# Kernel optimization log

Hardware: AMD Instinct MI355X
Metric: run time of the kernel (lower is better)

The kernel has to match this reference:

```python
import jax, jax.numpy as jnp
import numpy as np

STRIDE = (1, 1)
PAD = (1, 1)

def setup_inputs() -> dict:
    key = jax.random.key(0)
    k1, k2, k3 = jax.random.split(key, 3)
    x = jax.random.normal(k1, (32, 128, 56, 56), dtype=jnp.float32)
    # K ~ N(0,1) per nn.init.normal_(self.K)
    K = jax.random.normal(k2, (256, 128, 3, 3), dtype=jnp.float32)
    bias = jax.random.normal(k3, (1,), dtype=jnp.float32)  # single scalar bias added to whole output
    return {"x": x, "K": K, "bias": bias}

def reference(x, K, bias):
    # Cross-correlation (torch conv semantics), NCHW / OIHW, zero padding.
    y = jax.lax.conv_general_dilated(
        x, K,
        window_strides=STRIDE,
        padding=[(PAD[0], PAD[0]), (PAD[1], PAD[1])],
        dimension_numbers=("NCHW", "OIHW", "NCHW"),
    )
    # Original adds a single scalar bias to the entire output tensor.
    return y + bias
```

## Files before the change

kernel.cpp:

```cpp
#include <hip/hip_runtime.h>

typedef __bf16 bf16x8 __attribute__((ext_vector_type(8)));
typedef float  floatx4 __attribute__((ext_vector_type(4)));

#define HW   56
#define NPIX 3136
#define CIN  128
#define COUT 256

__global__ __launch_bounds__(256) void wt_transform_kernel(
        const float* __restrict__ Kw, __bf16* __restrict__ W2) {
    int idx = blockIdx.x * 256 + threadIdx.x;
    int ci    = idx & 31;
    int oc    = (idx >> 5) & 255;
    int tapcc = idx >> 13;
    int tap   = tapcc % 9;
    int cc    = tapcc / 9;
    int c = cc * 32 + ci;
    int r = tap / 3, s = tap % 3;
    W2[idx] = (__bf16)Kw[oc * 1152 + c * 9 + r * 3 + s];
}

__global__ __launch_bounds__(256) void conv_kernel(
        const float* __restrict__ x, const __bf16* __restrict__ W2,
        const float* __restrict__ bias, float* __restrict__ out) {
    __shared__ __align__(16) __bf16 Xs[4][66][32];

    const int t    = threadIdx.x;
    const int n    = blockIdx.x / 28;
    const int ht   = blockIdx.x % 28;
    const int h0   = ht * 2;
    const int ocb  = blockIdx.y * 128;

    const int wid  = t >> 6;
    const int lane = t & 63;
    const int quad = lane >> 4;
    const int l15  = lane & 15;

    floatx4 acc[2][8];
    #pragma unroll
    for (int mi = 0; mi < 2; ++mi)
        #pragma unroll
        for (int nj = 0; nj < 8; ++nj)
            acc[mi][nj] = (floatx4){0.f, 0.f, 0.f, 0.f};

    if (t < 160) {
        int pr = t >> 2;
        int zr = pr / 10;
        int zw = pr % 10;
        int wp = (zw == 0) ? 0 : (56 + zw);
        *(int4*)&Xs[zr][wp][(t & 3) * 8] = make_int4(0, 0, 0, 0);
    }

    const int q    = t >> 1;
    const int half = t & 1;
    const int srow = q & 3;
    const int sc   = q >> 2;
    const int hin  = h0 - 1 + srow;
    const bool hvalid = (unsigned)hin < 56u;

    for (int cc = 0; cc < 4; ++cc) {
        __syncthreads();
        const float* src = x + ((n * CIN + cc * 32 + sc) * NPIX) + hin * HW;
        #pragma unroll
        for (int j = 0; j < 7; ++j) {
            int w4 = (half * 7 + j) * 4;
            float4 v;
            if (hvalid) v = *(const float4*)(src + w4);
            else        v = make_float4(0.f, 0.f, 0.f, 0.f);
            Xs[srow][1 + w4 + 0][sc] = (__bf16)v.x;
            Xs[srow][1 + w4 + 1][sc] = (__bf16)v.y;
            Xs[srow][1 + w4 + 2][sc] = (__bf16)v.z;
            Xs[srow][1 + w4 + 3][sc] = (__bf16)v.w;
        }
        __syncthreads();

        #pragma unroll
        for (int tap = 0; tap < 9; ++tap) {
            const int r = tap / 3, s = tap % 3;
            const bf16x8* wb = (const bf16x8*)(W2 + (size_t)(cc * 9 + tap) * (256 * 32));
            bf16x8 afr[2];
            #pragma unroll
            for (int mi = 0; mi < 2; ++mi) {
                int oc = ocb + wid * 32 + mi * 16 + l15;
                afr[mi] = wb[oc * 4 + quad];
            }
            bf16x8 bfr[8];
            #pragma unroll
            for (int nj = 0; nj < 8; ++nj) {
                int p  = nj * 16 + l15;
                int pr = p >> 6;
                int pw = p & 63;
                bfr[nj] = *(const bf16x8*)&Xs[pr + r][pw + s][quad * 8];
            }
            #pragma unroll
            for (int mi = 0; mi < 2; ++mi)
                #pragma unroll
                for (int nj = 0; nj < 8; ++nj)
                    acc[mi][nj] = __builtin_amdgcn_mfma_f32_16x16x32_bf16(
                        afr[mi], bfr[nj], acc[mi][nj], 0, 0, 0);
        }
    }

    const float bv = bias[0];
    #pragma unroll
    for (int nj = 0; nj < 8; ++nj) {
        int p  = nj * 16 + l15;
        int pr = p >> 6;
        int pw = p & 63;
        if (pw < 56) {
            int hout = h0 + pr;
            #pragma unroll
            for (int mi = 0; mi < 2; ++mi) {
                int oc = ocb + wid * 32 + mi * 16 + quad * 4;
                float* o = out + ((n * COUT + oc) * NPIX) + hout * HW + pw;
                o[0 * NPIX] = acc[mi][nj].x + bv;
                o[1 * NPIX] = acc[mi][nj].y + bv;
                o[2 * NPIX] = acc[mi][nj].z + bv;
                o[3 * NPIX] = acc[mi][nj].w + bv;
            }
        }
    }
}

extern "C" void kernel_launch(void* const* d_in, const int* in_sizes, int n_in,
                              void* d_out, int out_size, void* d_ws, size_t ws_size,
                              hipStream_t stream) {
    const float* x    = (const float*)d_in[0];
    const float* Kw   = (const float*)d_in[1];
    const float* bias = (const float*)d_in[2];
    float* out = (float*)d_out;
    __bf16* W2 = (__bf16*)d_ws;

    wt_transform_kernel<<<dim3(1152), dim3(256), 0, stream>>>(Kw, W2);
    conv_kernel<<<dim3(32 * 28, 2), dim3(256), 0, stream>>>(x, W2, bias, out);
}
```

Measured before the change: 216.1 us.

## Switch to 32x32x16 MFMA with 4-row tiles and swizzled LDS staging

Each block now covers 4 output rows instead of 2, which halves the grid and cuts the redundant reloading of halo input rows. The MFMA moves from 16x16x32 to 32x32x16 with a 2x2 warp layout over output channels and pixels. The weight layout is re-packed into 8-channel groups to match. Input staging now writes vectorised 16-byte bf16 stores into an XOR-swizzled LDS layout, meant to avoid bank conflicts. This trades higher register pressure (launch bounds now request 2 blocks per CU) and strided per-channel global loads for better data reuse.

```diff
diff --git a/kernel.cpp b/kernel.cpp
--- a/kernel.cpp
+++ b/kernel.cpp
@@ -1,7 +1,7 @@
 #include <hip/hip_runtime.h>
 
 typedef __bf16 bf16x8 __attribute__((ext_vector_type(8)));
-typedef float  floatx4 __attribute__((ext_vector_type(4)));
+typedef float  floatx16 __attribute__((ext_vector_type(16)));
 
 #define HW   56
 #define NPIX 3136
@@ -11,113 +11,122 @@
 __global__ __launch_bounds__(256) void wt_transform_kernel(
         const float* __restrict__ Kw, __bf16* __restrict__ W2) {
     int idx = blockIdx.x * 256 + threadIdx.x;
-    int ci    = idx & 31;
-    int oc    = (idx >> 5) & 255;
+    int j     = idx & 7;
+    int oc    = (idx >> 3) & 255;
+    int cg    = (idx >> 11) & 3;
     int tapcc = idx >> 13;
     int tap   = tapcc % 9;
     int cc    = tapcc / 9;
-    int c = cc * 32 + ci;
-    int r = tap / 3, s = tap % 3;
-    W2[idx] = (__bf16)Kw[oc * 1152 + c * 9 + r * 3 + s];
+    int c = cc * 32 + cg * 8 + j;
+    W2[idx] = (__bf16)Kw[oc * 1152 + c * 9 + tap];
 }
 
-__global__ __launch_bounds__(256) void conv_kernel(
+__device__ __forceinline__ int xs_idx(int row, int wp, int cg) {
+    return row * 2112 + wp * 32 + ((cg ^ ((wp >> 1) & 3)) << 3);
+}
+
+__global__ __launch_bounds__(256, 2) void conv_kernel(
         const float* __restrict__ x, const __bf16* __restrict__ W2,
         const float* __restrict__ bias, float* __restrict__ out) {
-    __shared__ __align__(16) __bf16 Xs[4][66][32];
+    __shared__ __align__(16) __bf16 Xs[6 * 66 * 32];
 
     const int t    = threadIdx.x;
-    const int n    = blockIdx.x / 28;
-    const int ht   = blockIdx.x % 28;
-    const int h0   = ht * 2;
+    const int nb   = blockIdx.x / 14;
+    const int ht   = blockIdx.x % 14;
+    const int h0   = ht * 4;
     const int ocb  = blockIdx.y * 128;
 
     const int wid  = t >> 6;
     const int lane = t & 63;
-    const int quad = lane >> 4;
-    const int l15  = lane & 15;
+    const int half = lane >> 5;
+    const int l31  = lane & 31;
 
-    floatx4 acc[2][8];
+    const int oc_base = ocb + (wid & 1) * 64;
+    const int p_base  = (wid >> 1) * 128;
+
+    floatx16 acc[2][4];
     #pragma unroll
     for (int mi = 0; mi < 2; ++mi)
         #pragma unroll
-        for (int nj = 0; nj < 8; ++nj)
-            acc[mi][nj] = (floatx4){0.f, 0.f, 0.f, 0.f};
+        for (int nj = 0; nj < 4; ++nj)
+            #pragma unroll
+            for (int k = 0; k < 16; ++k)
+                acc[mi][nj][k] = 0.f;
 
-    if (t < 160) {
-        int pr = t >> 2;
-        int zr = pr / 10;
-        int zw = pr % 10;
-        int wp = (zw == 0) ? 0 : (56 + zw);
-        *(int4*)&Xs[zr][wp][(t & 3) * 8] = make_int4(0, 0, 0, 0);
+    if (t < 240) {
+        int cg   = t & 3;
+        int rest = t >> 2;
+        int row  = rest / 10;
+        int zw   = rest % 10;
+        int wp   = (zw == 0) ? 0 : (56 + zw);
+        *(int4*)&Xs[xs_idx(row, wp, cg)] = make_int4(0, 0, 0, 0);
     }
 
-    const int q    = t >> 1;
-    const int half = t & 1;
-    const int srow = q & 3;
-    const int sc   = q >> 2;
-    const int hin  = h0 - 1 + srow;
-    const bool hvalid = (unsigned)hin < 56u;
+    const int  sw     = t & 63;
+    const int  sg     = t >> 6;
+    const bool wvalid = sw < 56;
 
     for (int cc = 0; cc < 4; ++cc) {
         __syncthreads();
-        const float* src = x + ((n * CIN + cc * 32 + sc) * NPIX) + hin * HW;
-        #pragma unroll
-        for (int j = 0; j < 7; ++j) {
-            int w4 = (half * 7 + j) * 4;
-            float4 v;
-            if (hvalid) v = *(const float4*)(src + w4);
-            else        v = make_float4(0.f, 0.f, 0.f, 0.f);
-            Xs[srow][1 + w4 + 0][sc] = (__bf16)v.x;
-            Xs[srow][1 + w4 + 1][sc] = (__bf16)v.y;
-            Xs[srow][1 + w4 + 2][sc] = (__bf16)v.z;
-            Xs[srow][1 + w4 + 3][sc] = (__bf16)v.w;
+        for (int row = 0; row < 6; ++row) {
+            int hin = h0 - 1 + row;
+            bf16x8 v;
+            #pragma unroll
+            for (int j = 0; j < 8; ++j) v[j] = (__bf16)0.f;
+            if (wvalid && (unsigned)hin < 56u) {
+                const float* src = x + (size_t)(nb * CIN + cc * 32 + sg * 8) * NPIX
+                                     + hin * HW + sw;
+                #pragma unroll
+                for (int j = 0; j < 8; ++j)
+                    v[j] = (__bf16)src[j * NPIX];
+            }
+            if (wvalid)
+                *(bf16x8*)&Xs[xs_idx(row, 1 + sw, sg)] = v;
         }
         __syncthreads();
 
         #pragma unroll
         for (int tap = 0; tap < 9; ++tap) {
             const int r = tap / 3, s = tap % 3;
-            const bf16x8* wb = (const bf16x8*)(W2 + (size_t)(cc * 9 + tap) * (256 * 32));
-            bf16x8 afr[2];
+            const __bf16* wtap = W2 + (size_t)(cc * 9 + tap) * (4 * 256 * 8);
             #pragma unroll
-            for (int mi = 0; mi < 2; ++mi) {
-                int oc = ocb + wid * 32 + mi * 16 + l15;
-                afr[mi] = wb[oc * 4 + quad];
+            for (int kc = 0; kc < 2; ++kc) {
+                bf16x8 afr[2];
+                #pragma unroll
+                for (int mi = 0; mi < 2; ++mi) {
+                    int oc = oc_base + mi * 32 + l31;
+                    afr[mi] = *(const bf16x8*)(wtap + ((kc * 2 + half) * 256 + oc) * 8);
+                }
+                #pragma unroll
+                for (int nj = 0; nj < 4; ++nj) {
+                    int p  = p_base + nj * 32 + l31;
+                    int pr = p >> 6;
+                    int pw = p & 63;
+                    bf16x8 bfr = *(const bf16x8*)&Xs[xs_idx(pr + r, pw + s, kc * 2 + half)];
+                    #pragma unroll
+                    for (int mi = 0; mi < 2; ++mi)
+                        acc[mi][nj] = __builtin_amdgcn_mfma_f32_32x32x16_bf16(
+                            afr[mi], bfr, acc[mi][nj], 0, 0, 0);
+                }
             }
-            bf16x8 bfr[8];
-            #pragma unroll
-            for (int nj = 0; nj < 8; ++nj) {
-                int p  = nj * 16 + l15;
-                int pr = p >> 6;
-                int pw = p & 63;
-                bfr[nj] = *(const bf16x8*)&Xs[pr + r][pw + s][quad * 8];
-            }
-            #pragma unroll
-            for (int mi = 0; mi < 2; ++mi)
-                #pragma unroll
-                for (int nj = 0; nj < 8; ++nj)
-                    acc[mi][nj] = __builtin_amdgcn_mfma_f32_16x16x32_bf16(
-                        afr[mi], bfr[nj], acc[mi][nj], 0, 0, 0);
         }
     }
 
     const float bv = bias[0];
     #pragma unroll
-    for (int nj = 0; nj < 8; ++nj) {
-        int p  = nj * 16 + l15;
+    for (int nj = 0; nj < 4; ++nj) {
+        int p  = p_base + nj * 32 + l31;
         int pr = p >> 6;
         int pw = p & 63;
         if (pw < 56) {
             int hout = h0 + pr;
             #pragma unroll
             for (int mi = 0; mi < 2; ++mi) {
-                int oc = ocb + wid * 32 + mi * 16 + quad * 4;
-                float* o = out + ((n * COUT + oc) * NPIX) + hout * HW + pw;
-                o[0 * NPIX] = acc[mi][nj].x + bv;
-                o[1 * NPIX] = acc[mi][nj].y + bv;
-                o[2 * NPIX] = acc[mi][nj].z + bv;
-                o[3 * NPIX] = acc[mi][nj].w + bv;
+                #pragma unroll
+                for (int rg = 0; rg < 16; ++rg) {
+                    int oc = oc_base + mi * 32 + (rg & 3) + ((rg >> 2) << 3) + half * 4;
+                    out[(size_t)(nb * COUT + oc) * NPIX + hout * HW + pw] = acc[mi][nj][rg] + bv;
+                }
             }
         }
     }
@@ -133,5 +142,5 @@
     __bf16* W2 = (__bf16*)d_ws;
 
     wt_transform_kernel<<<dim3(1152), dim3(256), 0, stream>>>(Kw, W2);
-    conv_kernel<<<dim3(32 * 28, 2), dim3(256), 0, stream>>>(x, W2, bias, out);
+    conv_kernel<<<dim3(32 * 14, 2), dim3(256), 0, stream>>>(x, W2, bias, out);
 }
```

Result: faster. 209.3 us (-3.1%).
